# Kernel tuning notes

Hardware: AMD Instinct MI355X
Metric: run time of the kernel (lower is better)

## Reference

```python
import jax, jax.numpy as jnp
import numpy as np

B, L, D, H, K_DELAYS = 8, 2048, 512, 8, 8
DH = D // H


def setup_inputs() -> dict:
    key = jax.random.key(0)
    ks = jax.random.split(key, 6)
    def lin_w(k):
        return 0.02 * jax.random.normal(k, (D, D), jnp.float32)
    return {
        "x_q":  jax.random.normal(ks[0], (B, L, D), jnp.float32),
        "x_kv": jax.random.normal(ks[1], (B, L, D), jnp.float32),
        "Wq": lin_w(ks[2]), "bq": jnp.zeros((D,), jnp.float32),
        "Wk": lin_w(ks[3]), "bk": jnp.zeros((D,), jnp.float32),
        "Wv": lin_w(ks[4]), "bv": jnp.zeros((D,), jnp.float32),
        "Wo": lin_w(ks[5]), "bo": jnp.zeros((D,), jnp.float32),
    }


def reference(x_q, x_kv, Wq, bq, Wk, bk, Wv, bv, Wo, bo):
    Bx, Lx, Dx = x_q.shape

    def proj(x, W, b):  # torch Linear: x @ W.T + b, then split heads -> [B,H,L,dh]
        return (x @ W.T + b).reshape(Bx, Lx, H, DH).transpose(0, 2, 1, 3)

    q = proj(x_q, Wq, bq)
    k = proj(x_kv, Wk, bk)
    v = proj(x_kv, Wv, bv)

    # FFT-based autocorrelation over the time axis (axis=2)
    qz = q - q.mean(axis=2, keepdims=True)
    kz = k - k.mean(axis=2, keepdims=True)
    Qf = jnp.fft.rfft(qz, axis=2)
    Kf = jnp.fft.rfft(kz, axis=2)
    corr = jnp.fft.irfft(Qf * jnp.conj(Kf), n=Lx, axis=2).mean(axis=-1)  # [B,H,L]
    # torch expands corr to [B,H,Lq,Lk] then means over Lq -> identical to corr
    score = corr

    K = min(K_DELAYS, Lx)
    vals, idx = jax.lax.top_k(score, K)                    # [B,H,K]
    w = vals / (vals.sum(axis=-1, keepdims=True) + 1e-12)
    w = jax.lax.stop_gradient(w)                           # .detach() in torch

    # circular shift by -delay == gather at (t + delay) mod L
    t = jnp.arange(Lx)
    pos = (t[None, None, None, :] + idx[..., None]) % Lx   # [B,H,K,L]
    v_sh = jnp.take_along_axis(v[:, :, None, :, :], pos[..., None], axis=3)  # [B,H,K,L,dh]
    out = jnp.einsum('bhk,bhkld->bhld', w, v_sh)           # weighted sum over delays

    out = out.transpose(0, 2, 1, 3).reshape(Bx, Lx, Dx)
    return out @ Wo.T + bo
```

## Files before the change

kernel.cpp:

```cpp
#include <hip/hip_runtime.h>
#include <math.h>

#define BB 8
#define LL 2048
#define DD 512
#define HH 8
#define DHH 64
#define KD 8
#define MM (BB*LL)

typedef _Float16 f16x2 __attribute__((ext_vector_type(2)));
typedef _Float16 f16x4 __attribute__((ext_vector_type(4)));
typedef _Float16 f16x8 __attribute__((ext_vector_type(8)));
typedef float    f32x4 __attribute__((ext_vector_type(4)));

__device__ inline void cvt8(const float* __restrict__ s, _Float16* hp, _Float16* lp) {
    const float4 a = *(const float4*)s;
    const float4 b = *(const float4*)(s + 4);
    const float v[8] = {a.x, a.y, a.z, a.w, b.x, b.y, b.z, b.w};
    f16x8 hi, lo;
#pragma unroll
    for (int j = 0; j < 8; j++) {
        const _Float16 h = (_Float16)v[j];
        hi[j] = h;
        lo[j] = (_Float16)((v[j] - (float)h) * 512.0f);
    }
    *(f16x8*)hp = hi;
    if (lp) *(f16x8*)lp = lo;
}

__global__ __launch_bounds__(256) void prep_all(const float* __restrict__ xq,
                                                const float* __restrict__ xkv,
                                                const float* __restrict__ Wq, const float* __restrict__ Wk,
                                                const float* __restrict__ Wv, const float* __restrict__ Wo,
                                                _Float16* __restrict__ Xq_h, _Float16* __restrict__ Xq_l,
                                                _Float16* __restrict__ Xkv_h, _Float16* __restrict__ Xkv_l,
                                                _Float16* __restrict__ Wq_h, _Float16* __restrict__ Wq_l,
                                                _Float16* __restrict__ Wk_h, _Float16* __restrict__ Wk_l,
                                                _Float16* __restrict__ Wv_h, _Float16* __restrict__ Wo_h) {
    const int bid = blockIdx.x;
    if (bid < 8192) {
        const int g = bid * 256 + threadIdx.x;
        const int which = g >> 20;
        const size_t idx = (size_t)(g & 1048575) * 8;
        const float* src = which ? xkv : xq;
        _Float16* dh = which ? Xkv_h : Xq_h;
        _Float16* dl = which ? Xkv_l : Xq_l;
        cvt8(src + idx, dh + idx, dl + idx);
    } else {
        const int g = (bid - 8192) * 256 + threadIdx.x;
        const int which = g >> 15;
        const size_t idx = (size_t)(g & 32767) * 8;
        if (which == 0)      cvt8(Wq + idx, Wq_h + idx, Wq_l + idx);
        else if (which == 1) cvt8(Wk + idx, Wk_h + idx, Wk_l + idx);
        else if (which == 2) cvt8(Wv + idx, Wv_h + idx, nullptr);
        else                 cvt8(Wo + idx, Wo_h + idx, nullptr);
    }
}

__device__ __forceinline__ void stage16(const _Float16* g, const _Float16* l) {
    __builtin_amdgcn_global_load_lds(
        (const __attribute__((address_space(1))) void*)g,
        (__attribute__((address_space(3))) void*)l,
        16, 0, 0);
}

#define ASWZ(R, q) ((size_t)(R) * 32 + (size_t)((((q) ^ (((R) >> 1) & 3))) * 8))

template<int NPROD, int MODE>
__device__ __forceinline__ void gemm_body(const _Float16* __restrict__ Ag,
                                          const _Float16* __restrict__ Al_g,
                                          const _Float16* __restrict__ Bg,
                                          const _Float16* __restrict__ Bl_g,
                                          const float* __restrict__ bias,
                                          void* __restrict__ Cv,
                                          _Float16* lds, int l0) {
    _Float16* Ah = lds;
    _Float16* Bh = lds + 4096;
    _Float16* Al = (NPROD == 3) ? lds + 8192  : lds;
    _Float16* Bl = (NPROD == 3) ? lds + 12288 : lds;

    const int t  = threadIdx.x;
    const int m0 = (((l0 >> 5) << 3) | (l0 & 7)) * 128;
    const int n0 = ((l0 >> 3) & 3) * 128;

    const int wv   = t >> 6;
    const int lane = t & 63;
    const int wm   = (wv >> 1) * 64;
    const int wn   = (wv & 1) * 64;
    const int lm   = lane & 15;
    const int quad = lane >> 4;

    int srow[2], schk[2], sgrp[2];
#pragma unroll
    for (int i = 0; i < 2; i++) {
        const int s = (i * 4 + wv) * 64 + lane;
        srow[i] = s >> 2;
        schk[i] = (s & 3) ^ ((srow[i] >> 1) & 3);
        sgrp[i] = (i * 4 + wv) * 512;
    }

    f32x4 acc0[4][4] = {};
    f32x4 acc1[4][4] = {};

    for (int k0 = 0; k0 < 512; k0 += 32) {
        __syncthreads();
#pragma unroll
        for (int i = 0; i < 2; i++) {
            const size_t offA = (size_t)(m0 + srow[i]) * 512 + k0 + schk[i] * 8;
            const size_t offB = (size_t)(n0 + srow[i]) * 512 + k0 + schk[i] * 8;
            stage16(Ag + offA, Ah + sgrp[i]);
            stage16(Bg + offB, Bh + sgrp[i]);
            if (NPROD == 3) {
                stage16(Al_g + offA, Al + sgrp[i]);
                stage16(Bl_g + offB, Bl + sgrp[i]);
            }
        }
        __syncthreads();

        f16x8 afh[4], bf[4];
#pragma unroll
        for (int mt = 0; mt < 4; mt++)
            afh[mt] = *(f16x8*)&Ah[ASWZ(wm + mt * 16 + lm, quad)];
#pragma unroll
        for (int nt = 0; nt < 4; nt++)
            bf[nt] = *(f16x8*)&Bh[ASWZ(wn + nt * 16 + lm, quad)];

#pragma unroll
        for (int mt = 0; mt < 4; mt++)
#pragma unroll
            for (int nt = 0; nt < 4; nt++)
                acc0[mt][nt] = __builtin_amdgcn_mfma_f32_16x16x32_f16(afh[mt], bf[nt], acc0[mt][nt], 0, 0, 0);

        if (NPROD == 3) {
            f16x8 afl[4];
#pragma unroll
            for (int mt = 0; mt < 4; mt++)
                afl[mt] = *(f16x8*)&Al[ASWZ(wm + mt * 16 + lm, quad)];
#pragma unroll
            for (int mt = 0; mt < 4; mt++)
#pragma unroll
                for (int nt = 0; nt < 4; nt++)
                    acc1[mt][nt] = __builtin_amdgcn_mfma_f32_16x16x32_f16(afl[mt], bf[nt], acc1[mt][nt], 0, 0, 0);
#pragma unroll
            for (int nt = 0; nt < 4; nt++)
                bf[nt] = *(f16x8*)&Bl[ASWZ(wn + nt * 16 + lm, quad)];
#pragma unroll
            for (int mt = 0; mt < 4; mt++)
#pragma unroll
                for (int nt = 0; nt < 4; nt++)
                    acc1[mt][nt] = __builtin_amdgcn_mfma_f32_16x16x32_f16(afh[mt], bf[nt], acc1[mt][nt], 0, 0, 0);
        }
    }

#pragma unroll
    for (int mt = 0; mt < 4; mt++) {
#pragma unroll
        for (int nt = 0; nt < 4; nt++) {
            const int n = n0 + wn + nt * 16 + lm;
            const float bv = bias[n];
            float val[4];
#pragma unroll
            for (int r = 0; r < 4; r++) {
                val[r] = acc0[mt][nt][r] + bv;
                if (NPROD == 3) val[r] += acc1[mt][nt][r] * (1.0f / 512.0f);
            }
            const int mbase = m0 + wm + mt * 16 + quad * 4;
            const int b_idx = mbase >> 11;
            const int lbase = mbase & 2047;
            if (MODE == 0) {
                float* C = (float*)Cv;
#pragma unroll
                for (int r = 0; r < 4; r++) C[(size_t)(mbase + r) * 512 + n] = val[r];
            } else if (MODE == 1) {
                float* C = (float*)Cv;
                float4 pv = make_float4(val[0], val[1], val[2], val[3]);
                *(float4*)&C[((size_t)(b_idx * 512 + n)) * 2048 + lbase] = pv;
            } else {
                _Float16* C = (_Float16*)Cv;
#pragma unroll
                for (int r = 0; r < 4; r++)
                    C[(size_t)b_idx * 1048576 + (size_t)(n >> 6) * 131072
                      + (size_t)(lbase + r) * 64 + (n & 63)] = (_Float16)val[r];
            }
        }
    }
}

__global__ __launch_bounds__(256, 2) void gemm_qk(const _Float16* __restrict__ A0h, const _Float16* __restrict__ A0l,
                                                  const _Float16* __restrict__ B0h, const _Float16* __restrict__ B0l,
                                                  const float* __restrict__ bias0, float* __restrict__ C0,
                                                  const _Float16* __restrict__ A1h, const _Float16* __restrict__ A1l,
                                                  const _Float16* __restrict__ B1h, const _Float16* __restrict__ B1l,
                                                  const float* __restrict__ bias1, float* __restrict__ C1) {
    __shared__ __align__(16) _Float16 lds[16384];
    const int prob = blockIdx.x >> 9;
    const int l0   = blockIdx.x & 511;
    if (prob == 0)
        gemm_body<3, 1>(A0h, A0l, B0h, B0l, bias0, C0, lds, l0);
    else
        gemm_body<3, 1>(A1h, A1l, B1h, B1l, bias1, C1, lds, l0);
}

__global__ __launch_bounds__(256, 2) void gemm_o(const _Float16* __restrict__ Ah_g,
                                                 const _Float16* __restrict__ Bh_g,
                                                 const float* __restrict__ bias,
                                                 float* __restrict__ C) {
    __shared__ __align__(16) _Float16 lds[8192];
    gemm_body<1, 0>(Ah_g, Ah_g, Bh_g, Bh_g, bias, C, lds, blockIdx.x);
}

#define PAD3(i) ((i) + ((i) >> 3))

__device__ inline float2 cmul2(float2 a, float2 w) {
    return make_float2(a.x * w.x - a.y * w.y, a.x * w.y + a.y * w.x);
}
__device__ inline float2 cadd2(float2 a, float2 b) { return make_float2(a.x + b.x, a.y + b.y); }
__device__ inline float2 csub2(float2 a, float2 b) { return make_float2(a.x - b.x, a.y - b.y); }

__global__ __launch_bounds__(256) void fft_fwd(const float* __restrict__ qT,
                                               const float* __restrict__ kT,
                                               float* __restrict__ specP) {
    const int blk  = blockIdx.x;
    const int bh   = blk >> 4;
    const int part = blk & 15;
    const int t    = threadIdx.x;
    __shared__ float2 Zs[2304];
    __shared__ float2 Wt[1024];

#pragma unroll
    for (int s = 0; s < 4; s++) {
        const int j = t + s * 256;
        float sv, cv;
        __sincosf(2.0f * (float)M_PI * (float)j / 2048.0f, &sv, &cv);
        Wt[j] = make_float2(cv, -sv);
    }

    float2 pacc[8];
#pragma unroll
    for (int s = 0; s < 8; s++) pacc[s] = make_float2(0.0f, 0.0f);

    const int low5 = t & 31, hi3 = t >> 5;
    const int low2 = t & 3,  hi6 = t >> 2;

    float2 zn[8];
    {
        const int seq0 = bh * 64 + part * 4;
        const float* qp = qT + (size_t)seq0 * 2048;
        const float* kp = kT + (size_t)seq0 * 2048;
#pragma unroll
        for (int s = 0; s < 8; s++) zn[s] = make_float2(qp[t + 256 * s], kp[t + 256 * s]);
    }

    for (int j4 = 0; j4 < 4; j4++) {
        float2 z[8];
#pragma unroll
        for (int s = 0; s < 8; s++) z[s] = zn[s];
        if (j4 + 1 < 4) {
            const int seq = bh * 64 + part * 4 + j4 + 1;
            const float* qp = qT + (size_t)seq * 2048;
            const float* kp = kT + (size_t)seq * 2048;
#pragma unroll
            for (int s = 0; s < 8; s++) zn[s] = make_float2(qp[t + 256 * s], kp[t + 256 * s]);
        }
        __syncthreads();

#pragma unroll
        for (int sp = 0; sp < 4; sp++) {
            float2 u = z[sp], v = z[sp + 4];
            z[sp]     = cadd2(u, v);
            z[sp + 4] = cmul2(csub2(u, v), Wt[t + 256 * sp]);
        }
#pragma unroll
        for (int base = 0; base < 8; base += 4)
#pragma unroll
            for (int q2 = 0; q2 < 2; q2++) {
                float2 u = z[base + q2], v = z[base + q2 + 2];
                z[base + q2]     = cadd2(u, v);
                z[base + q2 + 2] = cmul2(csub2(u, v), Wt[2 * (t + 256 * q2)]);
            }
        {
            const float2 w = Wt[4 * t];
#pragma unroll
            for (int e = 0; e < 8; e += 2) {
                float2 u = z[e], v = z[e + 1];
                z[e]     = cadd2(u, v);
                z[e + 1] = cmul2(csub2(u, v), w);
            }
        }

#pragma unroll
        for (int s = 0; s < 8; s++) Zs[PAD3(t + 256 * s)] = z[s];
        __syncthreads();
#pragma unroll
        for (int s = 0; s < 8; s++) z[s] = Zs[PAD3(low5 + 32 * s + 256 * hi3)];

#pragma unroll
        for (int sp = 0; sp < 4; sp++) {
            float2 u = z[sp], v = z[sp + 4];
            z[sp]     = cadd2(u, v);
            z[sp + 4] = cmul2(csub2(u, v), Wt[8 * (low5 + 32 * sp)]);
        }
#pragma unroll
        for (int base = 0; base < 8; base += 4)
#pragma unroll
            for (int q2 = 0; q2 < 2; q2++) {
                float2 u = z[base + q2], v = z[base + q2 + 2];
                z[base + q2]     = cadd2(u, v);
                z[base + q2 + 2] = cmul2(csub2(u, v), Wt[16 * (low5 + 32 * q2)]);
            }
        {
            const float2 w = Wt[32 * low5];
#pragma unroll
            for (int e = 0; e < 8; e += 2) {
                float2 u = z[e], v = z[e + 1];
                z[e]     = cadd2(u, v);
                z[e + 1] = cmul2(csub2(u, v), w);
            }
        }

#pragma unroll
        for (int s = 0; s < 8; s++) Zs[PAD3(low5 + 32 * s + 256 * hi3)] = z[s];
        __syncthreads();
#pragma unroll
        for (int s = 0; s < 8; s++) z[s] = Zs[PAD3(low2 + 4 * s + 32 * hi6)];

#pragma unroll
        for (int sp = 0; sp < 4; sp++) {
            float2 u = z[sp], v = z[sp + 4];
            z[sp]     = cadd2(u, v);
            z[sp + 4] = cmul2(csub2(u, v), Wt[64 * (low2 + 4 * sp)]);
        }
#pragma unroll
        for (int base = 0; base < 8; base += 4)
#pragma unroll
            for (int q2 = 0; q2 < 2; q2++) {
                float2 u = z[base + q2], v = z[base + q2 + 2];
                z[base + q2]     = cadd2(u, v);
                z[base + q2 + 2] = cmul2(csub2(u, v), Wt[128 * (low2 + 4 * q2)]);
            }
        {
            const float2 w = Wt[256 * low2];
#pragma unroll
            for (int e = 0; e < 8; e += 2) {
                float2 u = z[e], v = z[e + 1];
                z[e]     = cadd2(u, v);
                z[e + 1] = cmul2(csub2(u, v), w);
            }
        }

#pragma unroll
        for (int s = 0; s < 8; s++) Zs[PAD3(low2 + 4 * s + 32 * hi6)] = z[s];
        __syncthreads();
#pragma unroll
        for (int s = 0; s < 8; s++) z[s] = Zs[PAD3(8 * t + s)];

#pragma unroll
        for (int base = 0; base < 8; base += 4) {
            {
                float2 u = z[base], v = z[base + 2];
                z[base]     = cadd2(u, v);
                z[base + 2] = csub2(u, v);
            }
            {
                float2 u = z[base + 1], v = z[base + 3];
                float2 d = csub2(u, v);
                z[base + 1] = cadd2(u, v);
                z[base + 3] = make_float2(d.y, -d.x);
            }
        }
#pragma unroll
        for (int e = 0; e < 8; e += 2) {
            float2 u = z[e], v = z[e + 1];
            z[e]     = cadd2(u, v);
            z[e + 1] = csub2(u, v);
        }

#pragma unroll
        for (int s = 0; s < 8; s++) Zs[PAD3(8 * t + s)] = z[s];
        __syncthreads();

#pragma unroll
        for (int s = 0; s < 8; s++) {
            const int p  = t + 256 * s;
            const int f  = (int)(__brev((unsigned)p) >> 21);
            const int fm = (2048 - f) & 2047;
            const int p2 = (int)(__brev((unsigned)fm) >> 21);
            const float2 zf = Zs[PAD3(p)];
            const float2 zm = Zs[PAD3(p2)];
            const float qr = 0.5f * (zf.x + zm.x);
            const float qi = 0.5f * (zf.y - zm.y);
            const float kr = 0.5f * (zf.y + zm.y);
            const float ki = 0.5f * (zm.x - zf.x);
            if (f != 0) {
                pacc[s].x += qr * kr + qi * ki;
                pacc[s].y += qi * kr - qr * ki;
            }
        }
    }

    float2* outp = (float2*)specP + (size_t)blk * 2048;
#pragma unroll
    for (int s = 0; s < 8; s++) outp[t + 256 * s] = pacc[s];
}

__device__ inline void build_twiddle(float2* Wt, int tid, float sign) {
#pragma unroll
    for (int s = 0; s < 4; s++) {
        const int j = tid + s * 256;
        const float a = 2.0f * (float)M_PI * (float)j / 2048.0f;
        float sv, cv;
        __sincosf(a, &sv, &cv);
        Wt[j] = make_float2(cv, sign * sv);
    }
}

__device__ inline void fft2048_stages(float2* Z, const float2* Wt, int tid) {
    for (int st = 0; st < 11; st++) {
        const int half = 1 << st;
        const int shift = 10 - st;
#pragma unroll
        for (int r = 0; r < 4; r++) {
            const int m   = tid + r * 256;
            const int grp = m >> st;
            const int pos = m & (half - 1);
            const int i0  = (grp << (st + 1)) + pos;
            const int i1  = i0 + half;
            const float2 w = Wt[pos << shift];
            const float2 a = Z[i0];
            const float2 b = Z[i1];
            const float tr = b.x * w.x - b.y * w.y;
            const float ti = b.x * w.y + b.y * w.x;
            Z[i0] = make_float2(a.x + tr, a.y + ti);
            Z[i1] = make_float2(a.x - tr, a.y - ti);
        }
        __syncthreads();
    }
}

__global__ __launch_bounds__(256, 2) void gemm_v_fftinv(const _Float16* __restrict__ Ah_g,
                                                        const _Float16* __restrict__ Bh_g,
                                                        const float* __restrict__ bias,
                                                        _Float16* __restrict__ C,
                                                        const float* __restrict__ specP,
                                                        int* __restrict__ delays,
                                                        float* __restrict__ weights) {
    __shared__ __align__(16) char smem[24608];
    const int bid = blockIdx.x;
    const int tid = threadIdx.x;

    if (bid >= 64) {
        gemm_body<1, 2>(Ah_g, Ah_g, Bh_g, Bh_g, bias, C, (_Float16*)smem, bid - 64);
        return;
    }

    const int bh = bid;
    float2* Z  = (float2*)smem;
    float2* Wt = (float2*)(smem + 16384);
    float*  wvs = (float*)(smem + 24576);
    int*    wis = (int*)(smem + 24592);

    build_twiddle(Wt, tid, +1.0f);

    const float2* sp = (const float2*)specP + (size_t)bh * 16 * 2048;
#pragma unroll
    for (int s = 0; s < 8; s++) {
        const int p = tid + s * 256;
        float2 acc = make_float2(0.0f, 0.0f);
#pragma unroll
        for (int part = 0; part < 16; part++) {
            const float2 v = sp[part * 2048 + p];
            acc.x += v.x; acc.y += v.y;
        }
        Z[p] = acc;
    }
    __syncthreads();
    fft2048_stages(Z, Wt, tid);

    const float scale = 1.0f / (2048.0f * 64.0f);
    float cv[8];
#pragma unroll
    for (int s = 0; s < 8; s++) cv[s] = Z[tid + s * 256].x * scale;

    float bkv[KD];
    int   bki[KD];
#pragma unroll
    for (int k = 0; k < KD; k++) {
        float lv = -1e30f;
        int   li = 1 << 30;
#pragma unroll
        for (int s = 0; s < 8; s++) {
            const int idx = tid + s * 256;
            if (cv[s] > lv || (cv[s] == lv && idx < li)) { lv = cv[s]; li = idx; }
        }
#pragma unroll
        for (int off = 1; off < 64; off <<= 1) {
            const float v2 = __shfl_xor(lv, off);
            const int   i2 = __shfl_xor(li, off);
            if (v2 > lv || (v2 == lv && i2 < li)) { lv = v2; li = i2; }
        }
        if ((tid & 63) == 0) { wvs[tid >> 6] = lv; wis[tid >> 6] = li; }
        __syncthreads();
        float bv = wvs[0];
        int   bi = wis[0];
#pragma unroll
        for (int j = 1; j < 4; j++) {
            const float v2 = wvs[j];
            const int   i2 = wis[j];
            if (v2 > bv || (v2 == bv && i2 < bi)) { bv = v2; bi = i2; }
        }
        bkv[k] = bv;
        bki[k] = bi;
        if ((bi & 255) == tid) {
            const int slot = bi >> 8;
#pragma unroll
            for (int s = 0; s < 8; s++)
                if (s == slot) cv[s] = -1e30f;
        }
        __syncthreads();
    }

    if (tid == 0) {
        float sum = 0.0f;
#pragma unroll
        for (int k = 0; k < KD; k++) sum += bkv[k];
        const float inv = 1.0f / (sum + 1e-12f);
#pragma unroll
        for (int k = 0; k < KD; k++) {
            weights[bh * KD + k] = bkv[k] * inv;
            delays[bh * KD + k]  = bki[k];
        }
    }
}

__global__ __launch_bounds__(256) void gather_ws(const _Float16* __restrict__ v,
                                                 const int* __restrict__ delays,
                                                 const float* __restrict__ weights,
                                                 _Float16* __restrict__ outb) {
    const int gp = blockIdx.x * 256 + threadIdx.x;
    const int c8 = gp & 63;
    const int m  = gp >> 6;
    const int l  = m & 2047;
    const int b  = m >> 11;
    const int ch = c8 * 8;
    const int h  = ch >> 6;
    const int dh = ch & 63;
    const int bh = b * 8 + h;

    const _Float16* vb = v + (size_t)bh * 131072;
    float a[8] = {};
#pragma unroll
    for (int k = 0; k < KD; k++) {
        const int   d = delays[bh * KD + k];
        const float w = weights[bh * KD + k];
        const int   p = (l + d) & 2047;
        const f16x8 pv = *(const f16x8*)&vb[p * 64 + dh];
#pragma unroll
        for (int j = 0; j < 8; j++) a[j] = fmaf(w, (float)pv[j], a[j]);
    }
    f16x8 ov;
#pragma unroll
    for (int j = 0; j < 8; j++) ov[j] = (_Float16)a[j];
    *(f16x8*)&outb[(size_t)m * 512 + ch] = ov;
}

extern "C" void kernel_launch(void* const* d_in, const int* in_sizes, int n_in,
                              void* d_out, int out_size, void* d_ws, size_t ws_size,
                              hipStream_t stream) {
    const float* x_q  = (const float*)d_in[0];
    const float* x_kv = (const float*)d_in[1];
    const float* Wq   = (const float*)d_in[2];
    const float* bq   = (const float*)d_in[3];
    const float* Wk   = (const float*)d_in[4];
    const float* bk   = (const float*)d_in[5];
    const float* Wv   = (const float*)d_in[6];
    const float* bv   = (const float*)d_in[7];
    const float* Wo   = (const float*)d_in[8];
    const float* bo   = (const float*)d_in[9];
    float* out = (float*)d_out;

    char* ws = (char*)d_ws;
    _Float16* Xq_h  = (_Float16*)(ws + 0);
    _Float16* Xq_l  = (_Float16*)(ws + 16777216);
    _Float16* Xkv_h = (_Float16*)(ws + 33554432);
    _Float16* Xkv_l = (_Float16*)(ws + 50331648);
    _Float16* Wq_h  = (_Float16*)(ws + 67108864);
    _Float16* Wq_l  = (_Float16*)(ws + 67633152);
    _Float16* Wk_h  = (_Float16*)(ws + 68157440);
    _Float16* Wk_l  = (_Float16*)(ws + 68681728);
    _Float16* Wv_h  = (_Float16*)(ws + 69206016);
    _Float16* Wo_h  = (_Float16*)(ws + 69730304);
    int*      dely  = (int*)    (ws + 70254592);
    float*    wgt   = (float*)  (ws + 70256640);
    float*    specP = (float*)  (ws + 50331648);
    _Float16* vh    = (_Float16*)(ws + 0);
    _Float16* gbuf  = (_Float16*)(ws + 16777216);
    float*    qf32  = (float*)d_out;

    const size_t kOff   = 70258688;
    const bool   merged = ws_size >= kOff + 33554432;
    float* kf32 = merged ? (float*)(ws + kOff) : (float*)(ws + 0);

    dim3 blk(256);

    prep_all<<<dim3(8704), blk, 0, stream>>>(x_q, x_kv, Wq, Wk, Wv, Wo,
                                             Xq_h, Xq_l, Xkv_h, Xkv_l,
                                             Wq_h, Wq_l, Wk_h, Wk_l, Wv_h, Wo_h);

    if (merged) {
        gemm_qk<<<dim3(1024), blk, 0, stream>>>(Xq_h, Xq_l, Wq_h, Wq_l, bq, qf32,
                                                Xkv_h, Xkv_l, Wk_h, Wk_l, bk, kf32);
    } else {
        gemm_qk<<<dim3(512), blk, 0, stream>>>(Xq_h, Xq_l, Wq_h, Wq_l, bq, qf32,
                                               Xq_h, Xq_l, Wq_h, Wq_l, bq, qf32);
        gemm_qk<<<dim3(512), blk, 0, stream>>>(Xkv_h, Xkv_l, Wk_h, Wk_l, bk, kf32,
                                               Xkv_h, Xkv_l, Wk_h, Wk_l, bk, kf32);
    }

    fft_fwd<<<dim3(1024), blk, 0, stream>>>(qf32, kf32, specP);

    gemm_v_fftinv<<<dim3(576), blk, 0, stream>>>(Xkv_h, Wv_h, bv, vh, specP, dely, wgt);

    gather_ws<<<dim3(4096), blk, 0, stream>>>(vh, dely, wgt, gbuf);

    gemm_o<<<dim3(512), blk, 0, stream>>>(gbuf, Wo_h, bo, out);
}
```

Measured before the change: 280.1 us.

## Fuse fp32-to-fp16 split conversion of activations into GEMM A-tile staging

```diff
diff --git a/kernel.cpp b/kernel.cpp
--- a/kernel.cpp
+++ b/kernel.cpp
@@ -29,33 +29,18 @@
     if (lp) *(f16x8*)lp = lo;
 }
 
-__global__ __launch_bounds__(256) void prep_all(const float* __restrict__ xq,
-                                                const float* __restrict__ xkv,
-                                                const float* __restrict__ Wq, const float* __restrict__ Wk,
-                                                const float* __restrict__ Wv, const float* __restrict__ Wo,
-                                                _Float16* __restrict__ Xq_h, _Float16* __restrict__ Xq_l,
-                                                _Float16* __restrict__ Xkv_h, _Float16* __restrict__ Xkv_l,
-                                                _Float16* __restrict__ Wq_h, _Float16* __restrict__ Wq_l,
-                                                _Float16* __restrict__ Wk_h, _Float16* __restrict__ Wk_l,
-                                                _Float16* __restrict__ Wv_h, _Float16* __restrict__ Wo_h) {
-    const int bid = blockIdx.x;
-    if (bid < 8192) {
-        const int g = bid * 256 + threadIdx.x;
-        const int which = g >> 20;
-        const size_t idx = (size_t)(g & 1048575) * 8;
-        const float* src = which ? xkv : xq;
-        _Float16* dh = which ? Xkv_h : Xq_h;
-        _Float16* dl = which ? Xkv_l : Xq_l;
-        cvt8(src + idx, dh + idx, dl + idx);
-    } else {
-        const int g = (bid - 8192) * 256 + threadIdx.x;
-        const int which = g >> 15;
-        const size_t idx = (size_t)(g & 32767) * 8;
-        if (which == 0)      cvt8(Wq + idx, Wq_h + idx, Wq_l + idx);
-        else if (which == 1) cvt8(Wk + idx, Wk_h + idx, Wk_l + idx);
-        else if (which == 2) cvt8(Wv + idx, Wv_h + idx, nullptr);
-        else                 cvt8(Wo + idx, Wo_h + idx, nullptr);
-    }
+__global__ __launch_bounds__(256) void prep_w(const float* __restrict__ Wq, const float* __restrict__ Wk,
+                                              const float* __restrict__ Wv, const float* __restrict__ Wo,
+                                              _Float16* __restrict__ Wq_h, _Float16* __restrict__ Wq_l,
+                                              _Float16* __restrict__ Wk_h, _Float16* __restrict__ Wk_l,
+                                              _Float16* __restrict__ Wv_h, _Float16* __restrict__ Wo_h) {
+    const int g = blockIdx.x * 256 + threadIdx.x;
+    const int which = g >> 15;
+    const size_t idx = (size_t)(g & 32767) * 8;
+    if (which == 0)      cvt8(Wq + idx, Wq_h + idx, Wq_l + idx);
+    else if (which == 1) cvt8(Wk + idx, Wk_h + idx, Wk_l + idx);
+    else if (which == 2) cvt8(Wv + idx, Wv_h + idx, nullptr);
+    else                 cvt8(Wo + idx, Wo_h + idx, nullptr);
 }
 
 __device__ __forceinline__ void stage16(const _Float16* g, const _Float16* l) {
@@ -67,8 +52,9 @@
 
 #define ASWZ(R, q) ((size_t)(R) * 32 + (size_t)((((q) ^ (((R) >> 1) & 3))) * 8))
 
-template<int NPROD, int MODE>
-__device__ __forceinline__ void gemm_body(const _Float16* __restrict__ Ag,
+template<int NPROD, int MODE, int AF32>
+__device__ __forceinline__ void gemm_body(const float* __restrict__ A32,
+                                          const _Float16* __restrict__ Ag,
                                           const _Float16* __restrict__ Al_g,
                                           const _Float16* __restrict__ Bg,
                                           const _Float16* __restrict__ Bl_g,
@@ -104,16 +90,37 @@
     f32x4 acc1[4][4] = {};
 
     for (int k0 = 0; k0 < 512; k0 += 32) {
+        float va[2][8];
+        if (AF32) {
+#pragma unroll
+            for (int i = 0; i < 2; i++) {
+                const float* src = A32 + (size_t)(m0 + srow[i]) * 512 + k0 + schk[i] * 8;
+                const float4 a = *(const float4*)src;
+                const float4 b = *(const float4*)(src + 4);
+                va[i][0] = a.x; va[i][1] = a.y; va[i][2] = a.z; va[i][3] = a.w;
+                va[i][4] = b.x; va[i][5] = b.y; va[i][6] = b.z; va[i][7] = b.w;
+            }
+        }
         __syncthreads();
 #pragma unroll
         for (int i = 0; i < 2; i++) {
-            const size_t offA = (size_t)(m0 + srow[i]) * 512 + k0 + schk[i] * 8;
             const size_t offB = (size_t)(n0 + srow[i]) * 512 + k0 + schk[i] * 8;
-            stage16(Ag + offA, Ah + sgrp[i]);
             stage16(Bg + offB, Bh + sgrp[i]);
-            if (NPROD == 3) {
-                stage16(Al_g + offA, Al + sgrp[i]);
-                stage16(Bl_g + offB, Bl + sgrp[i]);
+            if (NPROD == 3) stage16(Bl_g + offB, Bl + sgrp[i]);
+            if (AF32) {
+                f16x8 hi, lo;
+#pragma unroll
+                for (int j = 0; j < 8; j++) {
+                    const _Float16 h = (_Float16)va[i][j];
+                    hi[j] = h;
+                    if (NPROD == 3) lo[j] = (_Float16)((va[i][j] - (float)h) * 512.0f);
+                }
+                *(f16x8*)&Ah[sgrp[i] + lane * 8] = hi;
+                if (NPROD == 3) *(f16x8*)&Al[sgrp[i] + lane * 8] = lo;
+            } else {
+                const size_t offA = (size_t)(m0 + srow[i]) * 512 + k0 + schk[i] * 8;
+                stage16(Ag + offA, Ah + sgrp[i]);
+                if (NPROD == 3) stage16(Al_g + offA, Al + sgrp[i]);
             }
         }
         __syncthreads();
@@ -187,19 +194,19 @@
     }
 }
 
-__global__ __launch_bounds__(256, 2) void gemm_qk(const _Float16* __restrict__ A0h, const _Float16* __restrict__ A0l,
+__global__ __launch_bounds__(256, 2) void gemm_qk(const float* __restrict__ A0f,
                                                   const _Float16* __restrict__ B0h, const _Float16* __restrict__ B0l,
                                                   const float* __restrict__ bias0, float* __restrict__ C0,
-                                                  const _Float16* __restrict__ A1h, const _Float16* __restrict__ A1l,
+                                                  const float* __restrict__ A1f,
                                                   const _Float16* __restrict__ B1h, const _Float16* __restrict__ B1l,
                                                   const float* __restrict__ bias1, float* __restrict__ C1) {
     __shared__ __align__(16) _Float16 lds[16384];
     const int prob = blockIdx.x >> 9;
     const int l0   = blockIdx.x & 511;
     if (prob == 0)
-        gemm_body<3, 1>(A0h, A0l, B0h, B0l, bias0, C0, lds, l0);
+        gemm_body<3, 1, 1>(A0f, nullptr, nullptr, B0h, B0l, bias0, C0, lds, l0);
     else
-        gemm_body<3, 1>(A1h, A1l, B1h, B1l, bias1, C1, lds, l0);
+        gemm_body<3, 1, 1>(A1f, nullptr, nullptr, B1h, B1l, bias1, C1, lds, l0);
 }
 
 __global__ __launch_bounds__(256, 2) void gemm_o(const _Float16* __restrict__ Ah_g,
@@ -207,7 +214,7 @@
                                                  const float* __restrict__ bias,
                                                  float* __restrict__ C) {
     __shared__ __align__(16) _Float16 lds[8192];
-    gemm_body<1, 0>(Ah_g, Ah_g, Bh_g, Bh_g, bias, C, lds, blockIdx.x);
+    gemm_body<1, 0, 0>(nullptr, Ah_g, Ah_g, Bh_g, Bh_g, bias, C, lds, blockIdx.x);
 }
 
 #define PAD3(i) ((i) + ((i) >> 3))
@@ -438,7 +445,7 @@
     }
 }
 
-__global__ __launch_bounds__(256, 2) void gemm_v_fftinv(const _Float16* __restrict__ Ah_g,
+__global__ __launch_bounds__(256, 2) void gemm_v_fftinv(const float* __restrict__ xkv,
                                                         const _Float16* __restrict__ Bh_g,
                                                         const float* __restrict__ bias,
                                                         _Float16* __restrict__ C,
@@ -450,7 +457,7 @@
     const int tid = threadIdx.x;
 
     if (bid >= 64) {
-        gemm_body<1, 2>(Ah_g, Ah_g, Bh_g, Bh_g, bias, C, (_Float16*)smem, bid - 64);
+        gemm_body<1, 2, 1>(xkv, nullptr, nullptr, Bh_g, Bh_g, bias, C, (_Float16*)smem, bid - 64);
         return;
     }
 
@@ -580,46 +587,31 @@
     float* out = (float*)d_out;
 
     char* ws = (char*)d_ws;
-    _Float16* Xq_h  = (_Float16*)(ws + 0);
-    _Float16* Xq_l  = (_Float16*)(ws + 16777216);
-    _Float16* Xkv_h = (_Float16*)(ws + 33554432);
-    _Float16* Xkv_l = (_Float16*)(ws + 50331648);
-    _Float16* Wq_h  = (_Float16*)(ws + 67108864);
-    _Float16* Wq_l  = (_Float16*)(ws + 67633152);
-    _Float16* Wk_h  = (_Float16*)(ws + 68157440);
-    _Float16* Wk_l  = (_Float16*)(ws + 68681728);
-    _Float16* Wv_h  = (_Float16*)(ws + 69206016);
-    _Float16* Wo_h  = (_Float16*)(ws + 69730304);
-    int*      dely  = (int*)    (ws + 70254592);
-    float*    wgt   = (float*)  (ws + 70256640);
-    float*    specP = (float*)  (ws + 50331648);
-    _Float16* vh    = (_Float16*)(ws + 0);
-    _Float16* gbuf  = (_Float16*)(ws + 16777216);
+    float*    kf32  = (float*)   (ws + 0);
+    _Float16* vh    = (_Float16*)(ws + 33554432);
+    float*    specP = (float*)   (ws + 50331648);
+    _Float16* gbuf  = (_Float16*)(ws + 67108864);
+    _Float16* Wq_h  = (_Float16*)(ws + 83886080);
+    _Float16* Wq_l  = (_Float16*)(ws + 84410368);
+    _Float16* Wk_h  = (_Float16*)(ws + 84934656);
+    _Float16* Wk_l  = (_Float16*)(ws + 85458944);
+    _Float16* Wv_h  = (_Float16*)(ws + 85983232);
+    _Float16* Wo_h  = (_Float16*)(ws + 86507520);
+    int*      dely  = (int*)     (ws + 87031808);
+    float*    wgt   = (float*)   (ws + 87033856);
     float*    qf32  = (float*)d_out;
 
-    const size_t kOff   = 70258688;
-    const bool   merged = ws_size >= kOff + 33554432;
-    float* kf32 = merged ? (float*)(ws + kOff) : (float*)(ws + 0);
-
     dim3 blk(256);
 
-    prep_all<<<dim3(8704), blk, 0, stream>>>(x_q, x_kv, Wq, Wk, Wv, Wo,
-                                             Xq_h, Xq_l, Xkv_h, Xkv_l,
-                                             Wq_h, Wq_l, Wk_h, Wk_l, Wv_h, Wo_h);
-
-    if (merged) {
-        gemm_qk<<<dim3(1024), blk, 0, stream>>>(Xq_h, Xq_l, Wq_h, Wq_l, bq, qf32,
-                                                Xkv_h, Xkv_l, Wk_h, Wk_l, bk, kf32);
-    } else {
-        gemm_qk<<<dim3(512), blk, 0, stream>>>(Xq_h, Xq_l, Wq_h, Wq_l, bq, qf32,
-                                               Xq_h, Xq_l, Wq_h, Wq_l, bq, qf32);
-        gemm_qk<<<dim3(512), blk, 0, stream>>>(Xkv_h, Xkv_l, Wk_h, Wk_l, bk, kf32,
-                                               Xkv_h, Xkv_l, Wk_h, Wk_l, bk, kf32);
-    }
+    prep_w<<<dim3(512), blk, 0, stream>>>(Wq, Wk, Wv, Wo,
+                                          Wq_h, Wq_l, Wk_h, Wk_l, Wv_h, Wo_h);
+
+    gemm_qk<<<dim3(1024), blk, 0, stream>>>(x_q,  Wq_h, Wq_l, bq, qf32,
+                                            x_kv, Wk_h, Wk_l, bk, kf32);
 
     fft_fwd<<<dim3(1024), blk, 0, stream>>>(qf32, kf32, specP);
 
-    gemm_v_fftinv<<<dim3(576), blk, 0, stream>>>(Xkv_h, Wv_h, bv, vh, specP, dely, wgt);
+    gemm_v_fftinv<<<dim3(576), blk, 0, stream>>>(x_kv, Wv_h, bv, vh, specP, dely, wgt);
 
     gather_ws<<<dim3(4096), blk, 0, stream>>>(vh, dely, wgt, gbuf);
 
```

Result: faster. 272.9 us (-2.6%).
